# Kernel optimization log

Hardware: AMD Instinct MI355X
Metric: run time of the kernel (lower is better)

Reference implementation:

```python
import jax, jax.numpy as jnp
import numpy as np

HIDDEN = 4096
K = 4          # Gibbs sampling steps
LR = 0.01
IMG = (16, 64, 64, 3)  # batch, H, W, C


def setup_inputs() -> dict:
    key = jax.random.key(0)
    k1, k2 = jax.random.split(key)
    inputs = jax.random.uniform(k1, IMG, dtype=jnp.float32)
    flat = IMG[1] * IMG[2] * IMG[3]
    # GlorotNormal init: std = sqrt(2 / (fan_in + fan_out))
    scale = (2.0 / (flat + HIDDEN)) ** 0.5
    W = jax.random.normal(k2, (flat, HIDDEN), dtype=jnp.float32) * scale
    a = jnp.zeros((flat, 1), dtype=jnp.float32)
    b = jnp.zeros((HIDDEN, 1), dtype=jnp.float32)
    return {"inputs": inputs, "W": W, "a": a, "b": b}


def reference(inputs, W, a, b):
    B = inputs.shape[0]
    flat = inputs.shape[1] * inputs.shape[2] * inputs.shape[3]
    vs = inputs.reshape(B, flat, 1)  # each sample is a (flat,1) column vector

    def per_sample(carry, v):
        W, a, b = carry
        v_init = v
        # k Gibbs steps: h = sigma(b + W^T v); v = sigma(a + W h)
        h = None
        for _ in range(K):
            h = jax.nn.sigmoid(b + W.T @ v)
            v = jax.nn.sigmoid(a + W @ h)
        h_init = jax.nn.sigmoid(b + W.T @ v_init)
        # Contrastive divergence with .assign (replace, not accumulate) as in source
        W_new = LR * (v_init @ h_init.T - v @ h.T)
        a_new = LR * (v_init - v)
        b_new = LR * (h_init - h)
        return (W_new, a_new, b_new), v

    _, vs_out = jax.lax.scan(per_sample, (W, a, b), vs)
    # call() returns self.v, i.e. the reconstruction of the LAST batch element
    return vs_out[-1]
```

## Files before the change

kernel.cpp:

```cpp
#include <hip/hip_runtime.h>
#include <math.h>

#define FLAT 12288
#define NH   4096
#define KSTEPS 4
#define LRC 0.01f
#define NSEG 192
#define RPS  64

__device__ __forceinline__ float sigm(float x) {
    return __builtin_amdgcn_rcpf(1.0f + __expf(-x));
}

__device__ __forceinline__ unsigned short f2bf(float f) {
    unsigned u = __float_as_uint(f);
    unsigned r = u + 0x7FFFu + ((u >> 16) & 1u);
    return (unsigned short)(r >> 16);
}
__device__ __forceinline__ float bflo(unsigned w) { return __uint_as_float(w << 16); }
__device__ __forceinline__ float bfhi(unsigned w) { return __uint_as_float(w & 0xFFFF0000u); }

template <int CTRL>
__device__ __forceinline__ float dpp_add(float x) {
    int s = __builtin_amdgcn_update_dpp(0, __float_as_int(x), CTRL, 0xf, 0xf, true);
    return x + __int_as_float(s);
}
__device__ __forceinline__ float wave_sum63(float x) {
    x = dpp_add<0x111>(x);
    x = dpp_add<0x112>(x);
    x = dpp_add<0x114>(x);
    x = dpp_add<0x118>(x);
    x = dpp_add<0x142>(x);
    x = dpp_add<0x143>(x);
    return x;
}


__global__ __launch_bounds__(256) void k_colpart_cvt(const float* __restrict__ W,
                                                     const float* __restrict__ v,
                                                     float* __restrict__ partials,
                                                     unsigned short* __restrict__ Wbf) {
    const float4* W4 = (const float4*)W;
    int c4 = blockIdx.x * 256 + threadIdx.x;
    int r0 = blockIdx.y * RPS;
    float4 acc = make_float4(0.f, 0.f, 0.f, 0.f);
    for (int r = r0; r < r0 + RPS; ++r) {
        float vr = v[r];
        float4 w = W4[(size_t)r * (NH / 4) + c4];
        acc.x = fmaf(w.x, vr, acc.x);
        acc.y = fmaf(w.y, vr, acc.y);
        acc.z = fmaf(w.z, vr, acc.z);
        acc.w = fmaf(w.w, vr, acc.w);
        ushort4 bw;
        bw.x = f2bf(w.x); bw.y = f2bf(w.y); bw.z = f2bf(w.z); bw.w = f2bf(w.w);
        ((ushort4*)Wbf)[(size_t)r * (NH / 4) + c4] = bw;
    }
    ((float4*)partials)[(size_t)blockIdx.y * (NH / 4) + c4] = acc;
}

__global__ __launch_bounds__(256) void k_colpart_f32(const float* __restrict__ W,
                                                     const float* __restrict__ v,
                                                     float* __restrict__ partials) {
    const float4* W4 = (const float4*)W;
    int c4 = blockIdx.x * 256 + threadIdx.x;
    int r0 = blockIdx.y * RPS;
    float4 acc = make_float4(0.f, 0.f, 0.f, 0.f);
    for (int r = r0; r < r0 + RPS; ++r) {
        float vr = v[r];
        float4 w = W4[(size_t)r * (NH / 4) + c4];
        acc.x = fmaf(w.x, vr, acc.x);
        acc.y = fmaf(w.y, vr, acc.y);
        acc.z = fmaf(w.z, vr, acc.z);
        acc.w = fmaf(w.w, vr, acc.w);
    }
    ((float4*)partials)[(size_t)blockIdx.y * (NH / 4) + c4] = acc;
}

__global__ __launch_bounds__(256) void k_colpart_bf(const unsigned short* __restrict__ Wbf,
                                                    const float* __restrict__ v,
                                                    float* __restrict__ partials) {
    const uint4* W8 = (const uint4*)Wbf;
    int c8 = blockIdx.x * 256 + threadIdx.x;
    int r0 = blockIdx.y * RPS;
    float a0=0,a1=0,a2=0,a3=0,a4=0,a5=0,a6=0,a7=0;
    for (int r = r0; r < r0 + RPS; ++r) {
        float vr = v[r];
        uint4 w = W8[(size_t)r * (NH / 8) + c8];
        a0 = fmaf(bflo(w.x), vr, a0); a1 = fmaf(bfhi(w.x), vr, a1);
        a2 = fmaf(bflo(w.y), vr, a2); a3 = fmaf(bfhi(w.y), vr, a3);
        a4 = fmaf(bflo(w.z), vr, a4); a5 = fmaf(bfhi(w.z), vr, a5);
        a6 = fmaf(bflo(w.w), vr, a6); a7 = fmaf(bfhi(w.w), vr, a7);
    }
    float4* P = (float4*)(partials + (size_t)blockIdx.y * NH + (size_t)c8 * 8);
    float4 lo; lo.x=a0; lo.y=a1; lo.z=a2; lo.w=a3;
    float4 hi; hi.x=a4; hi.y=a5; hi.z=a6; hi.w=a7;
    P[0] = lo; P[1] = hi;
}

__global__ __launch_bounds__(256) void k_hreduce(const float* __restrict__ partials,
                                                 const float* __restrict__ b,
                                                 float* __restrict__ h,
                                                 float* __restrict__ hi) {
    int j = blockIdx.x * 256 + threadIdx.x;
    float s = 0.f;
    for (int g = 0; g < NSEG; ++g) s += partials[(size_t)g * NH + j];
    float hh = sigm(s + b[j]);
    h[j] = hh;
    if (hi) hi[j] = hh;
}

__global__ __launch_bounds__(256) void k_vstep_bf(const unsigned short* __restrict__ Wbf,
                                                  const float* __restrict__ h,
                                                  const float* __restrict__ a,
                                                  float* __restrict__ v) {
    int wid = threadIdx.x >> 6, lane = threadIdx.x & 63;
    int row = blockIdx.x * 4 + wid;
    const uint4* Wr = (const uint4*)(Wbf + (size_t)row * NH);
    const float4* h4 = (const float4*)h;
    float acc = 0.f;
    for (int k = lane; k < NH / 8; k += 64) {
        uint4 w = Wr[k];
        float4 ha = h4[2 * k], hb = h4[2 * k + 1];
        acc = fmaf(bflo(w.x), ha.x, acc); acc = fmaf(bfhi(w.x), ha.y, acc);
        acc = fmaf(bflo(w.y), ha.z, acc); acc = fmaf(bfhi(w.y), ha.w, acc);
        acc = fmaf(bflo(w.z), hb.x, acc); acc = fmaf(bfhi(w.z), hb.y, acc);
        acc = fmaf(bflo(w.w), hb.z, acc); acc = fmaf(bfhi(w.w), hb.w, acc);
    }
    acc = wave_sum63(acc);
    if (lane == 63) v[row] = sigm(a[row] + acc);
}

__global__ __launch_bounds__(256) void k_vstep_f32(const float* __restrict__ W,
                                                   const float* __restrict__ h,
                                                   const float* __restrict__ a,
                                                   float* __restrict__ v) {
    int wid = threadIdx.x >> 6, lane = threadIdx.x & 63;
    int row = blockIdx.x * 4 + wid;
    const float4* Wr = (const float4*)(W + (size_t)row * NH);
    const float4* h4 = (const float4*)h;
    float acc = 0.f;
    for (int k = lane; k < NH / 4; k += 64) {
        float4 w = Wr[k];
        float4 hh = h4[k];
        acc = fmaf(w.x, hh.x, fmaf(w.y, hh.y, fmaf(w.z, hh.z, fmaf(w.w, hh.w, acc))));
    }
    acc = wave_sum63(acc);
    if (lane == 63) v[row] = sigm(a[row] + acc);
}


#define TB  512
#define RVB (FLAT / TB)
#define RHB (NH / TB)
#define NWAVES (TB / 64)

__global__ __launch_bounds__(512) void k_phaseB(const float* __restrict__ inputs,
                                                const float* __restrict__ hi0,
                                                const float* __restrict__ hk0,
                                                const float* __restrict__ vk0,
                                                float* __restrict__ out) {
    int t = threadIdx.x;
    int lane = t & 63, wid = t >> 6;
    __shared__ float2 red[2][NWAVES];

    float Vi[RVB], Vk[RVB], v[RVB];
    float Hi[RHB], Hk[RHB], h[RHB], hini[RHB];

#pragma unroll
    for (int r = 0; r < RVB; r++) { int i = r * TB + t; Vi[r] = inputs[i]; Vk[r] = vk0[i]; }
#pragma unroll
    for (int r = 0; r < RHB; r++) { int j = r * TB + t; Hi[r] = hi0[j]; Hk[r] = hk0[j]; }

    int rc = 0;
    for (int s = 1; s < 16; ++s) {
        const float* vin = inputs + (size_t)s * FLAT;
#pragma unroll
        for (int r = 0; r < RVB; r++) v[r] = vin[r * TB + t];

        for (int k = 0; k < KSTEPS; ++k) {
            float px = 0.f, py = 0.f;
#pragma unroll
            for (int r = 0; r < RVB; r++) { px = fmaf(Vi[r], v[r], px); py = fmaf(Vk[r], v[r], py); }
            px = wave_sum63(px); py = wave_sum63(py);
            if (lane == 63) { float2 w2; w2.x = px; w2.y = py; red[rc & 1][wid] = w2; }
            __syncthreads();
            float al = 0.f, be = 0.f;
#pragma unroll
            for (int w = 0; w < NWAVES; w++) { float2 w2 = red[rc & 1][w]; al += w2.x; be += w2.y; }
            rc++;
            float ca = LRC * (1.f + al), cb = LRC * (1.f + be);

            float qx = 0.f, qy = 0.f;
#pragma unroll
            for (int r = 0; r < RHB; r++) {
                float hh = sigm(ca * Hi[r] - cb * Hk[r]);
                h[r] = hh;
                if (k == 0) hini[r] = hh;
                qx = fmaf(Hi[r], hh, qx); qy = fmaf(Hk[r], hh, qy);
            }
            qx = wave_sum63(qx); qy = wave_sum63(qy);
            if (lane == 63) { float2 w2; w2.x = qx; w2.y = qy; red[rc & 1][wid] = w2; }
            __syncthreads();
            float ga = 0.f, de = 0.f;
#pragma unroll
            for (int w = 0; w < NWAVES; w++) { float2 w2 = red[rc & 1][w]; ga += w2.x; de += w2.y; }
            rc++;
            float cg = LRC * (1.f + ga), cd = LRC * (1.f + de);

#pragma unroll
            for (int r = 0; r < RVB; r++) v[r] = sigm(cg * Vi[r] - cd * Vk[r]);
        }

#pragma unroll
        for (int r = 0; r < RVB; r++) { Vk[r] = v[r]; Vi[r] = vin[r * TB + t]; }
#pragma unroll
        for (int r = 0; r < RHB; r++) { Hk[r] = h[r]; Hi[r] = hini[r]; }
    }

#pragma unroll
    for (int r = 0; r < RVB; r++) out[r * TB + t] = Vk[r];
}


extern "C" void kernel_launch(void* const* d_in, const int* in_sizes, int n_in,
                              void* d_out, int out_size, void* d_ws, size_t ws_size,
                              hipStream_t stream) {
    const float* inputs = (const float*)d_in[0];
    const float* W      = (const float*)d_in[1];
    const float* a_in   = (const float*)d_in[2];
    const float* b_in   = (const float*)d_in[3];
    float* out = (float*)d_out;

    const size_t WBF_BYTES = (size_t)FLAT * NH * sizeof(unsigned short);
    const size_t TAIL_FLOATS = (size_t)NSEG * NH + NH + NH + FLAT;
    bool use_bf16 = ws_size >= WBF_BYTES + TAIL_FLOATS * sizeof(float) + 256;

    dim3 blk(256);
    if (use_bf16) {
        unsigned short* Wbf = (unsigned short*)d_ws;
        float* partials = (float*)((char*)d_ws + WBF_BYTES);
        float* h  = partials + (size_t)NSEG * NH;
        float* hi = h + NH;
        float* v  = hi + NH;

        k_colpart_cvt<<<dim3(4, NSEG), blk, 0, stream>>>(W, inputs, partials, Wbf);
        k_hreduce<<<dim3(NH / 256), blk, 0, stream>>>(partials, b_in, h, hi);
        k_vstep_bf<<<dim3(FLAT / 4), blk, 0, stream>>>(Wbf, h, a_in, v);
        for (int k = 1; k < KSTEPS; ++k) {
            k_colpart_bf<<<dim3(2, NSEG), blk, 0, stream>>>(Wbf, v, partials);
            k_hreduce<<<dim3(NH / 256), blk, 0, stream>>>(partials, b_in, h, (float*)nullptr);
            k_vstep_bf<<<dim3(FLAT / 4), blk, 0, stream>>>(Wbf, h, a_in, v);
        }
        k_phaseB<<<1, TB, 0, stream>>>(inputs, hi, h, v, out);
    } else {
        float* partials = (float*)d_ws;
        float* h  = partials + (size_t)NSEG * NH;
        float* hi = h + NH;
        float* v  = hi + NH;

        k_colpart_f32<<<dim3(4, NSEG), blk, 0, stream>>>(W, inputs, partials);
        k_hreduce<<<dim3(NH / 256), blk, 0, stream>>>(partials, b_in, h, hi);
        k_vstep_f32<<<dim3(FLAT / 4), blk, 0, stream>>>(W, h, a_in, v);
        for (int k = 1; k < KSTEPS; ++k) {
            k_colpart_f32<<<dim3(4, NSEG), blk, 0, stream>>>(W, v, partials);
            k_hreduce<<<dim3(NH / 256), blk, 0, stream>>>(partials, b_in, h, (float*)nullptr);
            k_vstep_f32<<<dim3(FLAT / 4), blk, 0, stream>>>(W, h, a_in, v);
        }
        k_phaseB<<<1, TB, 0, stream>>>(inputs, hi, h, v, out);
    }
}
```

Measured before the change: 547.7 us.

## Store weight copy as scaled FP8 instead of bf16 for Gibbs matvecs

New measurement: 537.7 us. No clear change (-1.8%).

```diff
diff --git a/kernel.cpp b/kernel.cpp
--- a/kernel.cpp
+++ b/kernel.cpp
@@ -5,20 +5,16 @@
 #define NH   4096
 #define KSTEPS 4
 #define LRC 0.01f
-#define NSEG 192
-#define RPS  64
+#define NSEG 384
+#define RPS  32
+#define WSCALE 64.0f
+#define WINV   0.015625f
+
+typedef float v2f __attribute__((ext_vector_type(2)));
 
 __device__ __forceinline__ float sigm(float x) {
     return __builtin_amdgcn_rcpf(1.0f + __expf(-x));
 }
-
-__device__ __forceinline__ unsigned short f2bf(float f) {
-    unsigned u = __float_as_uint(f);
-    unsigned r = u + 0x7FFFu + ((u >> 16) & 1u);
-    return (unsigned short)(r >> 16);
-}
-__device__ __forceinline__ float bflo(unsigned w) { return __uint_as_float(w << 16); }
-__device__ __forceinline__ float bfhi(unsigned w) { return __uint_as_float(w & 0xFFFF0000u); }
 
 template <int CTRL>
 __device__ __forceinline__ float dpp_add(float x) {
@@ -39,7 +35,7 @@
 __global__ __launch_bounds__(256) void k_colpart_cvt(const float* __restrict__ W,
                                                      const float* __restrict__ v,
                                                      float* __restrict__ partials,
-                                                     unsigned short* __restrict__ Wbf) {
+                                                     unsigned int* __restrict__ W8) {
     const float4* W4 = (const float4*)W;
     int c4 = blockIdx.x * 256 + threadIdx.x;
     int r0 = blockIdx.y * RPS;
@@ -51,101 +47,89 @@
         acc.y = fmaf(w.y, vr, acc.y);
         acc.z = fmaf(w.z, vr, acc.z);
         acc.w = fmaf(w.w, vr, acc.w);
-        ushort4 bw;
-        bw.x = f2bf(w.x); bw.y = f2bf(w.y); bw.z = f2bf(w.z); bw.w = f2bf(w.w);
-        ((ushort4*)Wbf)[(size_t)r * (NH / 4) + c4] = bw;
+        unsigned int p = 0;
+        p = __builtin_amdgcn_cvt_pk_fp8_f32(w.x * WSCALE, w.y * WSCALE, p, false);
+        p = __builtin_amdgcn_cvt_pk_fp8_f32(w.z * WSCALE, w.w * WSCALE, p, true);
+        W8[(size_t)r * (NH / 4) + c4] = p;
     }
     ((float4*)partials)[(size_t)blockIdx.y * (NH / 4) + c4] = acc;
 }
 
-__global__ __launch_bounds__(256) void k_colpart_f32(const float* __restrict__ W,
+__global__ __launch_bounds__(256) void k_colpart_fp8(const uint4* __restrict__ W8,
                                                      const float* __restrict__ v,
                                                      float* __restrict__ partials) {
-    const float4* W4 = (const float4*)W;
-    int c4 = blockIdx.x * 256 + threadIdx.x;
-    int r0 = blockIdx.y * RPS;
-    float4 acc = make_float4(0.f, 0.f, 0.f, 0.f);
+    int c16 = threadIdx.x;
+    int r0 = blockIdx.x * RPS;
+    float acc[16];
+#pragma unroll
+    for (int i = 0; i < 16; i++) acc[i] = 0.f;
     for (int r = r0; r < r0 + RPS; ++r) {
-        float vr = v[r];
-        float4 w = W4[(size_t)r * (NH / 4) + c4];
-        acc.x = fmaf(w.x, vr, acc.x);
-        acc.y = fmaf(w.y, vr, acc.y);
-        acc.z = fmaf(w.z, vr, acc.z);
-        acc.w = fmaf(w.w, vr, acc.w);
-    }
-    ((float4*)partials)[(size_t)blockIdx.y * (NH / 4) + c4] = acc;
-}
-
-__global__ __launch_bounds__(256) void k_colpart_bf(const unsigned short* __restrict__ Wbf,
-                                                    const float* __restrict__ v,
-                                                    float* __restrict__ partials) {
-    const uint4* W8 = (const uint4*)Wbf;
-    int c8 = blockIdx.x * 256 + threadIdx.x;
-    int r0 = blockIdx.y * RPS;
-    float a0=0,a1=0,a2=0,a3=0,a4=0,a5=0,a6=0,a7=0;
-    for (int r = r0; r < r0 + RPS; ++r) {
-        float vr = v[r];
-        uint4 w = W8[(size_t)r * (NH / 8) + c8];
-        a0 = fmaf(bflo(w.x), vr, a0); a1 = fmaf(bfhi(w.x), vr, a1);
-        a2 = fmaf(bflo(w.y), vr, a2); a3 = fmaf(bfhi(w.y), vr, a3);
-        a4 = fmaf(bflo(w.z), vr, a4); a5 = fmaf(bfhi(w.z), vr, a5);
-        a6 = fmaf(bflo(w.w), vr, a6); a7 = fmaf(bfhi(w.w), vr, a7);
-    }
-    float4* P = (float4*)(partials + (size_t)blockIdx.y * NH + (size_t)c8 * 8);
-    float4 lo; lo.x=a0; lo.y=a1; lo.z=a2; lo.w=a3;
-    float4 hi; hi.x=a4; hi.y=a5; hi.z=a6; hi.w=a7;
-    P[0] = lo; P[1] = hi;
+        float vr = v[r] * WINV;
+        uint4 w = W8[(size_t)r * (NH / 16) + c16];
+        v2f f;
+        f = __builtin_amdgcn_cvt_pk_f32_fp8(w.x, false); acc[0]  = fmaf(f.x, vr, acc[0]);  acc[1]  = fmaf(f.y, vr, acc[1]);
+        f = __builtin_amdgcn_cvt_pk_f32_fp8(w.x, true);  acc[2]  = fmaf(f.x, vr, acc[2]);  acc[3]  = fmaf(f.y, vr, acc[3]);
+        f = __builtin_amdgcn_cvt_pk_f32_fp8(w.y, false); acc[4]  = fmaf(f.x, vr, acc[4]);  acc[5]  = fmaf(f.y, vr, acc[5]);
+        f = __builtin_amdgcn_cvt_pk_f32_fp8(w.y, true);  acc[6]  = fmaf(f.x, vr, acc[6]);  acc[7]  = fmaf(f.y, vr, acc[7]);
+        f = __builtin_amdgcn_cvt_pk_f32_fp8(w.z, false); acc[8]  = fmaf(f.x, vr, acc[8]);  acc[9]  = fmaf(f.y, vr, acc[9]);
+        f = __builtin_amdgcn_cvt_pk_f32_fp8(w.z, true);  acc[10] = fmaf(f.x, vr, acc[10]); acc[11] = fmaf(f.y, vr, acc[11]);
+        f = __builtin_amdgcn_cvt_pk_f32_fp8(w.w, false); acc[12] = fmaf(f.x, vr, acc[12]); acc[13] = fmaf(f.y, vr, acc[13]);
+        f = __builtin_amdgcn_cvt_pk_f32_fp8(w.w, true);  acc[14] = fmaf(f.x, vr, acc[14]); acc[15] = fmaf(f.y, vr, acc[15]);
+    }
+    float4* P = (float4*)(partials + (size_t)blockIdx.x * NH + (size_t)c16 * 16);
+#pragma unroll
+    for (int q = 0; q < 4; q++) {
+        float4 o; o.x = acc[4*q]; o.y = acc[4*q+1]; o.z = acc[4*q+2]; o.w = acc[4*q+3];
+        P[q] = o;
+    }
 }
 
 __global__ __launch_bounds__(256) void k_hreduce(const float* __restrict__ partials,
                                                  const float* __restrict__ b,
                                                  float* __restrict__ h,
                                                  float* __restrict__ hi) {
-    int j = blockIdx.x * 256 + threadIdx.x;
+    int c  = threadIdx.x & 31;
+    int sg = threadIdx.x >> 5;
+    int col = blockIdx.x * 32 + c;
     float s = 0.f;
-    for (int g = 0; g < NSEG; ++g) s += partials[(size_t)g * NH + j];
-    float hh = sigm(s + b[j]);
-    h[j] = hh;
-    if (hi) hi[j] = hh;
-}
-
-__global__ __launch_bounds__(256) void k_vstep_bf(const unsigned short* __restrict__ Wbf,
-                                                  const float* __restrict__ h,
-                                                  const float* __restrict__ a,
-                                                  float* __restrict__ v) {
-    int wid = threadIdx.x >> 6, lane = threadIdx.x & 63;
-    int row = blockIdx.x * 4 + wid;
-    const uint4* Wr = (const uint4*)(Wbf + (size_t)row * NH);
-    const float4* h4 = (const float4*)h;
-    float acc = 0.f;
-    for (int k = lane; k < NH / 8; k += 64) {
-        uint4 w = Wr[k];
-        float4 ha = h4[2 * k], hb = h4[2 * k + 1];
-        acc = fmaf(bflo(w.x), ha.x, acc); acc = fmaf(bfhi(w.x), ha.y, acc);
-        acc = fmaf(bflo(w.y), ha.z, acc); acc = fmaf(bfhi(w.y), ha.w, acc);
-        acc = fmaf(bflo(w.z), hb.x, acc); acc = fmaf(bfhi(w.z), hb.y, acc);
-        acc = fmaf(bflo(w.w), hb.z, acc); acc = fmaf(bfhi(w.w), hb.w, acc);
-    }
-    acc = wave_sum63(acc);
-    if (lane == 63) v[row] = sigm(a[row] + acc);
-}
-
-__global__ __launch_bounds__(256) void k_vstep_f32(const float* __restrict__ W,
+    for (int g = sg; g < NSEG; g += 8) s += partials[(size_t)g * NH + col];
+    __shared__ float red[8][33];
+    red[sg][c] = s;
+    __syncthreads();
+    if (threadIdx.x < 32) {
+        float t = 0.f;
+#pragma unroll
+        for (int g2 = 0; g2 < 8; g2++) t += red[g2][threadIdx.x];
+        float hh = sigm(t + b[col]);
+        h[col] = hh;
+        if (hi) hi[col] = hh;
+    }
+}
+
+__global__ __launch_bounds__(256) void k_vstep_fp8(const unsigned char* __restrict__ W8,
                                                    const float* __restrict__ h,
                                                    const float* __restrict__ a,
                                                    float* __restrict__ v) {
     int wid = threadIdx.x >> 6, lane = threadIdx.x & 63;
     int row = blockIdx.x * 4 + wid;
-    const float4* Wr = (const float4*)(W + (size_t)row * NH);
+    const uint4* Wr = (const uint4*)(W8 + (size_t)row * NH);
     const float4* h4 = (const float4*)h;
     float acc = 0.f;
-    for (int k = lane; k < NH / 4; k += 64) {
-        float4 w = Wr[k];
-        float4 hh = h4[k];
-        acc = fmaf(w.x, hh.x, fmaf(w.y, hh.y, fmaf(w.z, hh.z, fmaf(w.w, hh.w, acc))));
+    for (int k = lane; k < NH / 16; k += 64) {
+        uint4 w = Wr[k];
+        float4 h0 = h4[4*k], h1 = h4[4*k+1], h2 = h4[4*k+2], h3 = h4[4*k+3];
+        v2f f;
+        f = __builtin_amdgcn_cvt_pk_f32_fp8(w.x, false); acc = fmaf(f.x, h0.x, acc); acc = fmaf(f.y, h0.y, acc);
+        f = __builtin_amdgcn_cvt_pk_f32_fp8(w.x, true);  acc = fmaf(f.x, h0.z, acc); acc = fmaf(f.y, h0.w, acc);
+        f = __builtin_amdgcn_cvt_pk_f32_fp8(w.y, false); acc = fmaf(f.x, h1.x, acc); acc = fmaf(f.y, h1.y, acc);
+        f = __builtin_amdgcn_cvt_pk_f32_fp8(w.y, true);  acc = fmaf(f.x, h1.z, acc); acc = fmaf(f.y, h1.w, acc);
+        f = __builtin_amdgcn_cvt_pk_f32_fp8(w.z, false); acc = fmaf(f.x, h2.x, acc); acc = fmaf(f.y, h2.y, acc);
+        f = __builtin_amdgcn_cvt_pk_f32_fp8(w.z, true);  acc = fmaf(f.x, h2.z, acc); acc = fmaf(f.y, h2.w, acc);
+        f = __builtin_amdgcn_cvt_pk_f32_fp8(w.w, false); acc = fmaf(f.x, h3.x, acc); acc = fmaf(f.y, h3.y, acc);
+        f = __builtin_amdgcn_cvt_pk_f32_fp8(w.w, true);  acc = fmaf(f.x, h3.z, acc); acc = fmaf(f.y, h3.w, acc);
     }
     acc = wave_sum63(acc);
-    if (lane == 63) v[row] = sigm(a[row] + acc);
+    if (lane == 63) v[row] = sigm(a[row] + acc * WINV);
 }
 
 
@@ -178,10 +162,13 @@
         for (int r = 0; r < RVB; r++) v[r] = vin[r * TB + t];
 
         for (int k = 0; k < KSTEPS; ++k) {
-            float px = 0.f, py = 0.f;
-#pragma unroll
-            for (int r = 0; r < RVB; r++) { px = fmaf(Vi[r], v[r], px); py = fmaf(Vk[r], v[r], py); }
-            px = wave_sum63(px); py = wave_sum63(py);
+            float px0 = 0.f, px1 = 0.f, py0 = 0.f, py1 = 0.f;
+#pragma unroll
+            for (int r = 0; r < RVB; r += 2) {
+                px0 = fmaf(Vi[r],   v[r],   px0); py0 = fmaf(Vk[r],   v[r],   py0);
+                px1 = fmaf(Vi[r+1], v[r+1], px1); py1 = fmaf(Vk[r+1], v[r+1], py1);
+            }
+            float px = wave_sum63(px0 + px1), py = wave_sum63(py0 + py1);
             if (lane == 63) { float2 w2; w2.x = px; w2.y = py; red[rc & 1][wid] = w2; }
             __syncthreads();
             float al = 0.f, be = 0.f;
@@ -231,41 +218,23 @@
     const float* b_in   = (const float*)d_in[3];
     float* out = (float*)d_out;
 
-    const size_t WBF_BYTES = (size_t)FLAT * NH * sizeof(unsigned short);
-    const size_t TAIL_FLOATS = (size_t)NSEG * NH + NH + NH + FLAT;
-    bool use_bf16 = ws_size >= WBF_BYTES + TAIL_FLOATS * sizeof(float) + 256;
+    unsigned int* W8 = (unsigned int*)d_ws;
+    float* partials = (float*)((char*)d_ws + (size_t)FLAT * NH);
+    float* h  = partials + (size_t)NSEG * NH;
+    float* hi = h + NH;
+    float* v  = hi + NH;
 
     dim3 blk(256);
-    if (use_bf16) {
-        unsigned short* Wbf = (unsigned short*)d_ws;
-        float* partials = (float*)((char*)d_ws + WBF_BYTES);
-        float* h  = partials + (size_t)NSEG * NH;
-        float* hi = h + NH;
-        float* v  = hi + NH;
-
-        k_colpart_cvt<<<dim3(4, NSEG), blk, 0, stream>>>(W, inputs, partials, Wbf);
-        k_hreduce<<<dim3(NH / 256), blk, 0, stream>>>(partials, b_in, h, hi);
-        k_vstep_bf<<<dim3(FLAT / 4), blk, 0, stream>>>(Wbf, h, a_in, v);
-        for (int k = 1; k < KSTEPS; ++k) {
-            k_colpart_bf<<<dim3(2, NSEG), blk, 0, stream>>>(Wbf, v, partials);
-            k_hreduce<<<dim3(NH / 256), blk, 0, stream>>>(partials, b_in, h, (float*)nullptr);
-            k_vstep_bf<<<dim3(FLAT / 4), blk, 0, stream>>>(Wbf, h, a_in, v);
-        }
-        k_phaseB<<<1, TB, 0, stream>>>(inputs, hi, h, v, out);
-    } else {
-        float* partials = (float*)d_ws;
-        float* h  = partials + (size_t)NSEG * NH;
-        float* hi = h + NH;
-        float* v  = hi + NH;
-
-        k_colpart_f32<<<dim3(4, NSEG), blk, 0, stream>>>(W, inputs, partials);
-        k_hreduce<<<dim3(NH / 256), blk, 0, stream>>>(partials, b_in, h, hi);
-        k_vstep_f32<<<dim3(FLAT / 4), blk, 0, stream>>>(W, h, a_in, v);
-        for (int k = 1; k < KSTEPS; ++k) {
-            k_colpart_f32<<<dim3(4, NSEG), blk, 0, stream>>>(W, v, partials);
-            k_hreduce<<<dim3(NH / 256), blk, 0, stream>>>(partials, b_in, h, (float*)nullptr);
-            k_vstep_f32<<<dim3(FLAT / 4), blk, 0, stream>>>(W, h, a_in, v);
-        }
-        k_phaseB<<<1, TB, 0, stream>>>(inputs, hi, h, v, out);
-    }
-}
+
+    k_colpart_cvt<<<dim3(4, NSEG), blk, 0, stream>>>(W, inputs, partials, W8);
+    k_hreduce<<<dim3(NH / 32), blk, 0, stream>>>(partials, b_in, h, hi);
+    k_vstep_fp8<<<dim3(FLAT / 4), blk, 0, stream>>>((const unsigned char*)W8, h, a_in, v);
+
+    for (int k = 1; k < KSTEPS; ++k) {
+        k_colpart_fp8<<<dim3(NSEG), blk, 0, stream>>>((const uint4*)W8, v, partials);
+        k_hreduce<<<dim3(NH / 32), blk, 0, stream>>>(partials, b_in, h, (float*)nullptr);
+        k_vstep_fp8<<<dim3(FLAT / 4), blk, 0, stream>>>((const unsigned char*)W8, h, a_in, v);
+    }
+
+    k_phaseB<<<1, TB, 0, stream>>>(inputs, hi, h, v, out);
+}
```
